# Performance work log

Measured on AMD Instinct MI355X. Metric: run time of the kernel, lower is better.

Reference implementation:

```python
import jax, jax.numpy as jnp
import numpy as np

T, B = 256, 64
X_DIM, H_DIM, Z_DIM = 128, 1024, 128


def _lin(k, out_d, in_d):
    return jax.random.normal(k, (out_d, in_d), jnp.float32) * 0.05


def setup_inputs() -> dict:
    key = jax.random.key(0)
    ks = jax.random.split(key, 18)
    return {
        "x": jax.random.normal(ks[0], (T, B, X_DIM), jnp.float32),
        "y": jax.random.uniform(ks[1], (T, B, X_DIM), jnp.float32),
        "eps": jax.random.normal(ks[2], (T, B, Z_DIM), jnp.float32),
        # hidden_state_rnn: GRU(x_dim -> h_dim), bias=False
        "h_Wih": _lin(ks[3], 3 * H_DIM, X_DIM),
        "h_Whh": _lin(ks[4], 3 * H_DIM, H_DIM),
        # rnn: GRU(h_dim + x_dim -> h_dim), bias=False (input is [y_t, h_t])
        "a_Wih": _lin(ks[5], 3 * H_DIM, X_DIM + H_DIM),
        "a_Whh": _lin(ks[6], 3 * H_DIM, H_DIM),
        "enc_W1": _lin(ks[7], H_DIM, H_DIM), "enc_b1": jnp.zeros(H_DIM, jnp.float32),
        "enc_W2": _lin(ks[8], H_DIM, H_DIM), "enc_b2": jnp.zeros(H_DIM, jnp.float32),
        "encm_W": _lin(ks[9], Z_DIM, H_DIM), "encm_b": jnp.zeros(Z_DIM, jnp.float32),
        "encs_W": _lin(ks[10], Z_DIM, H_DIM), "encs_b": jnp.zeros(Z_DIM, jnp.float32),
        "pr_W": _lin(ks[11], H_DIM, H_DIM), "pr_b": jnp.zeros(H_DIM, jnp.float32),
        "prm_W": _lin(ks[12], Z_DIM, H_DIM), "prm_b": jnp.zeros(Z_DIM, jnp.float32),
        "prs_W": _lin(ks[13], Z_DIM, H_DIM), "prs_b": jnp.zeros(Z_DIM, jnp.float32),
        "dec_W1": _lin(ks[14], H_DIM, H_DIM + Z_DIM), "dec_b1": jnp.zeros(H_DIM, jnp.float32),
        "dec_W2": _lin(ks[15], H_DIM, H_DIM), "dec_b2": jnp.zeros(H_DIM, jnp.float32),
        "decm_W": _lin(ks[16], X_DIM, H_DIM), "decm_b": jnp.zeros(X_DIM, jnp.float32),
        "decs_W": _lin(ks[17], X_DIM, H_DIM), "decs_b": jnp.zeros(X_DIM, jnp.float32),
    }


def _gru(xs, Wih, Whh):
    """Single-layer PyTorch-style GRU without biases. xs: [T,B,in]. Returns [T,B,H]."""
    h0 = jnp.zeros((xs.shape[1], Whh.shape[1]), xs.dtype)
    def step(h, xt):
        gi = xt @ Wih.T                      # [B, 3H]
        gh = h @ Whh.T                       # [B, 3H]
        ir, iz, inn = jnp.split(gi, 3, axis=-1)
        hr, hz, hn = jnp.split(gh, 3, axis=-1)
        r = jax.nn.sigmoid(ir + hr)
        zg = jax.nn.sigmoid(iz + hz)
        n = jnp.tanh(inn + r * hn)
        h_new = (1.0 - zg) * n + zg * h
        return h_new, h_new
    return jax.lax.scan(step, h0, xs)[1]


def srnn_forward(x, y, eps, h_Wih, h_Whh, a_Wih, a_Whh,
                 enc_W1, enc_b1, enc_W2, enc_b2, encm_W, encm_b, encs_W, encs_b,
                 pr_W, pr_b, prm_W, prm_b, prs_W, prs_b,
                 dec_W1, dec_b1, dec_W2, dec_b2, decm_W, decm_b, decs_W, decs_b):
    h_seq = _gru(x, h_Wih, h_Whh)            # [T,B,H] forward-time states
    # NOTE: original code aliases h_list and reverses it in place, so all later
    # uses of h_list[t] actually see the time-reversed sequence. Reproduce that.
    h_rev = h_seq[::-1]
    y_rev = y[::-1]
    a_rev = _gru(jnp.concatenate([y_rev, h_rev], axis=-1), a_Wih, a_Whh)  # backward GRU
    a_fwd = a_rev[::-1]                      # a at forward time t saw steps t..T-1

    enc = jax.nn.relu(jax.nn.relu(a_fwd @ enc_W1.T + enc_b1) @ enc_W2.T + enc_b2)
    enc_mean = enc @ encm_W.T + encm_b       # [T,B,Z]
    enc_std = jax.nn.softplus(enc @ encs_W.T + encs_b)
    z = eps * enc_std + enc_mean             # reparameterized sample

    pri = jax.nn.relu(h_rev @ pr_W.T + pr_b)  # bug-faithful: reversed h
    prior_mean = pri @ prm_W.T + prm_b
    prior_std = jax.nn.softplus(pri @ prs_W.T + prs_b)

    dec = jax.nn.relu(
        jax.nn.relu(jnp.concatenate([z, h_rev], axis=-1) @ dec_W1.T + dec_b1)
        @ dec_W2.T + dec_b2)
    dec_mean = jax.nn.sigmoid(dec @ decm_W.T + decm_b)  # [T,B,X]
    dec_std = jax.nn.softplus(dec @ decs_W.T + decs_b)

    kld = 0.5 * jnp.sum(
        2.0 * jnp.log(prior_std) - 2.0 * jnp.log(enc_std)
        + (enc_std ** 2 + (enc_mean - prior_mean) ** 2) / prior_std ** 2 - 1.0)
    nll = -jnp.sum(y * jnp.log(dec_mean) + (1.0 - y) * jnp.log(1.0 - dec_mean))
    return kld, nll, enc_mean, enc_std, dec_mean, dec_std


def reference(x, y, eps, h_Wih, h_Whh, a_Wih, a_Whh,
              enc_W1, enc_b1, enc_W2, enc_b2, encm_W, encm_b, encs_W, encs_b,
              pr_W, pr_b, prm_W, prm_b, prs_W, prs_b,
              dec_W1, dec_b1, dec_W2, dec_b2, decm_W, decm_b, decs_W, decs_b):
    return srnn_forward(x, y, eps, h_Wih, h_Whh, a_Wih, a_Whh,
                        enc_W1, enc_b1, enc_W2, enc_b2, encm_W, encm_b, encs_W, encs_b,
                        pr_W, pr_b, prm_W, prm_b, prs_W, prs_b,
                        dec_W1, dec_b1, dec_W2, dec_b2, decm_W, decm_b, decs_W, decs_b)
```

## Files before the change

kernel.cpp:

```cpp
#include <hip/hip_runtime.h>
#include <cstdint>
#include <cstddef>

#define NT   256
#define NB   64
#define XD   128
#define HD   1024
#define ZD   128
#define H3   3072
#define TBM  16384

typedef __attribute__((ext_vector_type(8))) short bf16x8;
typedef __attribute__((ext_vector_type(4))) float f32x4;
typedef __attribute__((ext_vector_type(4))) unsigned int u32x4;

__device__ __forceinline__ unsigned short f2bf(float f){
  unsigned int u = __float_as_uint(f);
  u += 0x7fffu + ((u >> 16) & 1u);
  return (unsigned short)(u >> 16);
}
__device__ __forceinline__ float bf2f(unsigned short h){
  return __uint_as_float(((unsigned int)h) << 16);
}

template<int N>
__device__ __forceinline__ void vwait(){
  asm volatile("s_waitcnt vmcnt(%0)" :: "i"(N) : "memory");
  __builtin_amdgcn_sched_barrier(0);
}

__device__ __forceinline__ float fsigmoid(float x){
  return 1.f / (1.f + __expf(-x));
}
__device__ __forceinline__ float ftanh(float x){
  float xc = fminf(fmaxf(x, -15.f), 15.f);
  float e = __expf(2.f * xc);
  return (e - 1.f) / (e + 1.f);
}

__device__ __forceinline__ void wait_tags(const unsigned int* tags, unsigned int target){
  if (threadIdx.x < 64){
    const unsigned int* p = tags + threadIdx.x * 32;
    for (;;){
      unsigned int v;
      asm volatile("global_load_dword %0, %1, off sc0 sc1\n\ts_waitcnt vmcnt(0)"
                   : "=v"(v) : "v"(p) : "memory");
      if (__all((int)(v >= target))) break;
    }
  }
  __syncthreads();
}

struct CvtArgs { const float* src[17]; };

__global__ void cvt_all(CvtArgs a, unsigned short* wdst, unsigned short* xdst, unsigned short* ydst){
  const long NG = 2572288;
  for (long g = blockIdx.x*blockDim.x + threadIdx.x; g < NG; g += (long)gridDim.x*blockDim.x){
    long i = g * 8;
    const float* s; unsigned short* d;
    if      (i < 393216)  { s=a.src[0]+i;             d=wdst+i; }
    else if (i < 3538944) { s=a.src[1]+(i-393216);    d=wdst+i; }
    else if (i < 7077888) { s=a.src[2]+(i-3538944);   d=wdst+i; }
    else if (i < 10223616){ s=a.src[3]+(i-7077888);   d=wdst+i; }
    else if (i < 11272192){ s=a.src[4]+(i-10223616);  d=wdst+i; }
    else if (i < 12320768){ s=a.src[5]+(i-11272192);  d=wdst+i; }
    else if (i < 12451840){ s=a.src[6]+(i-12320768);  d=wdst+i; }
    else if (i < 12582912){ s=a.src[7]+(i-12451840);  d=wdst+i; }
    else if (i < 13631488){ s=a.src[8]+(i-12582912);  d=wdst+i; }
    else if (i < 13762560){ s=a.src[9]+(i-13631488);  d=wdst+i; }
    else if (i < 13893632){ s=a.src[10]+(i-13762560); d=wdst+i; }
    else if (i < 15073280){ s=a.src[11]+(i-13893632); d=wdst+i; }
    else if (i < 16121856){ s=a.src[12]+(i-15073280); d=wdst+i; }
    else if (i < 16252928){ s=a.src[13]+(i-16121856); d=wdst+i; }
    else if (i < 16384000){ s=a.src[14]+(i-16252928); d=wdst+i; }
    else if (i < 18481152){ s=a.src[15]+(i-16384000); d=xdst+(i-16384000); }
    else                  { s=a.src[16]+(i-18481152); d=ydst+(i-18481152); }
    float4 v0 = *(const float4*)s;
    float4 v1 = *(const float4*)(s + 4);
    u32x4 o;
    o.x = (unsigned int)f2bf(v0.x) | ((unsigned int)f2bf(v0.y) << 16);
    o.y = (unsigned int)f2bf(v0.z) | ((unsigned int)f2bf(v0.w) << 16);
    o.z = (unsigned int)f2bf(v1.x) | ((unsigned int)f2bf(v1.y) << 16);
    o.w = (unsigned int)f2bf(v1.z) | ((unsigned int)f2bf(v1.w) << 16);
    *(u32x4*)d = o;
  }
}

template<int ACT, int OUT_BF, int BIAS>
__launch_bounds__(256)
__global__ void gemm_bf16(const unsigned short* __restrict__ A1, int rev1, int K1,
                          const unsigned short* __restrict__ A2, int rev2, int K,
                          const unsigned short* __restrict__ W,
                          const float* __restrict__ bias,
                          void* __restrict__ Cv, int N, int m0)
{
  __shared__ __align__(16) unsigned short As[128][40];
  __shared__ __align__(16) unsigned short Ws[128][40];
  const int tid   = threadIdx.x;
  const int mbase = blockIdx.y * 128;
  const int nbase = blockIdx.x * 128;
  const int wid = tid >> 6, lane = tid & 63;
  const int wr = wid >> 1, wc = wid & 1;
  const int fr = lane & 15;
  const int kc = (lane >> 4) * 8;
  const int K2 = K - K1;
  const int nk = K >> 5;

  f32x4 acc[4][4];
  #pragma unroll
  for (int i = 0; i < 4; ++i)
    #pragma unroll
    for (int j = 0; j < 4; ++j)
      acc[i][j] = (f32x4){0.f, 0.f, 0.f, 0.f};

  for (int ks = 0; ks < nk; ++ks){
    const int k0 = ks << 5;
    __syncthreads();
    for (int l = tid; l < 512; l += 256){
      int row = l >> 2, c = l & 3;
      int kk = k0 + c*8;
      int m = m0 + mbase + row;
      uint4 v;
      if (kk < K1){
        int mm = rev1 ? (((255 - (m >> 6)) << 6) | (m & 63)) : m;
        v = *(const uint4*)(A1 + (size_t)mm * K1 + kk);
      } else {
        int mm = rev2 ? (((255 - (m >> 6)) << 6) | (m & 63)) : m;
        v = *(const uint4*)(A2 + (size_t)mm * K2 + (kk - K1));
      }
      *(uint4*)&As[row][c*8] = v;
    }
    for (int l = tid; l < 512; l += 256){
      int row = l >> 2, c = l & 3;
      uint4 v = *(const uint4*)(W + (size_t)(nbase + row) * K + k0 + c*8);
      *(uint4*)&Ws[row][c*8] = v;
    }
    __syncthreads();
    bf16x8 af[4], bfm[4];
    #pragma unroll
    for (int f = 0; f < 4; ++f) af[f]  = *(const bf16x8*)&As[wr*64 + f*16 + fr][kc];
    #pragma unroll
    for (int f = 0; f < 4; ++f) bfm[f] = *(const bf16x8*)&Ws[wc*64 + f*16 + fr][kc];
    #pragma unroll
    for (int i = 0; i < 4; ++i)
      #pragma unroll
      for (int j = 0; j < 4; ++j)
        acc[i][j] = __builtin_amdgcn_mfma_f32_16x16x32_bf16(af[i], bfm[j], acc[i][j], 0, 0, 0);
  }

  #pragma unroll
  for (int i = 0; i < 4; ++i){
    #pragma unroll
    for (int j = 0; j < 4; ++j){
      #pragma unroll
      for (int r = 0; r < 4; ++r){
        int row = mbase + wr*64 + i*16 + (lane >> 4)*4 + r;
        int col = nbase + wc*64 + j*16 + fr;
        float v = acc[i][j][r];
        if (BIAS) v += bias[col];
        if (ACT == 1) v = fmaxf(v, 0.f);
        else if (ACT == 2) v = 1.f / (1.f + expf(-v));
        else if (ACT == 3) v = (v > 20.f) ? v : log1pf(expf(v));
        if (OUT_BF) ((unsigned short*)Cv)[(size_t)row * N + col] = f2bf(v);
        else        ((float*)Cv)[(size_t)row * N + col] = v;
      }
    }
  }
}

__device__ void gemm_gi_tile(char* smem,
                             const unsigned short* __restrict__ A1, int rev1, int K1,
                             const unsigned short* __restrict__ A2, int rev2, int K,
                             const unsigned short* __restrict__ W,
                             unsigned short* __restrict__ C, int m0, int bx, int by)
{
  unsigned short (*As)[40] = (unsigned short(*)[40])smem;
  unsigned short (*Ws)[40] = (unsigned short(*)[40])(smem + 10240);
  const int tid   = threadIdx.x;
  const int mbase = by * 128;
  const int nbase = bx * 128;
  const int wid = tid >> 6, lane = tid & 63;
  const int wr = wid >> 1, wc = wid & 1;
  const int fr = lane & 15;
  const int kc = (lane >> 4) * 8;
  const int K2 = K - K1;
  const int nk = K >> 5;

  f32x4 acc[4][4];
  #pragma unroll
  for (int i = 0; i < 4; ++i)
    #pragma unroll
    for (int j = 0; j < 4; ++j)
      acc[i][j] = (f32x4){0.f, 0.f, 0.f, 0.f};

  for (int ks = 0; ks < nk; ++ks){
    const int k0 = ks << 5;
    __syncthreads();
    for (int l = tid; l < 512; l += 256){
      int row = l >> 2, c = l & 3;
      int kk = k0 + c*8;
      int m = m0 + mbase + row;
      uint4 v;
      if (kk < K1){
        int mm = rev1 ? (((255 - (m >> 6)) << 6) | (m & 63)) : m;
        v = *(const uint4*)(A1 + (size_t)mm * K1 + kk);
      } else {
        int mm = rev2 ? (((255 - (m >> 6)) << 6) | (m & 63)) : m;
        v = *(const uint4*)(A2 + (size_t)mm * K2 + (kk - K1));
      }
      *(uint4*)&As[row][c*8] = v;
    }
    for (int l = tid; l < 512; l += 256){
      int row = l >> 2, c = l & 3;
      uint4 v = *(const uint4*)(W + (size_t)(nbase + row) * K + k0 + c*8);
      *(uint4*)&Ws[row][c*8] = v;
    }
    __syncthreads();
    bf16x8 af[4], bfm[4];
    #pragma unroll
    for (int f = 0; f < 4; ++f) af[f]  = *(const bf16x8*)&As[wr*64 + f*16 + fr][kc];
    #pragma unroll
    for (int f = 0; f < 4; ++f) bfm[f] = *(const bf16x8*)&Ws[wc*64 + f*16 + fr][kc];
    #pragma unroll
    for (int i = 0; i < 4; ++i)
      #pragma unroll
      for (int j = 0; j < 4; ++j)
        acc[i][j] = __builtin_amdgcn_mfma_f32_16x16x32_bf16(af[i], bfm[j], acc[i][j], 0, 0, 0);
  }

  #pragma unroll
  for (int i = 0; i < 4; ++i){
    #pragma unroll
    for (int j = 0; j < 4; ++j){
      #pragma unroll
      for (int r = 0; r < 4; ++r){
        int row = mbase + wr*64 + i*16 + (lane >> 4)*4 + r;
        int col = nbase + wc*64 + j*16 + fr;
        C[(size_t)row * H3 + col] = f2bf(acc[i][j][r]);
      }
    }
  }
  __syncthreads();
}

__device__ void gru_body(char* smem,
                         const unsigned short* __restrict__ W3,
                         const unsigned short* __restrict__ gi,
                         unsigned short* __restrict__ seq,
                         float* __restrict__ hstate,
                         unsigned int* __restrict__ tags,
                         int t0, int dir, int out_off, int nsteps)
{
  uint4 (*Wf)[3][64] = (uint4(*)[3][64])smem;
  unsigned short (*hb2)[16] = (unsigned short(*)[16])(smem + 98304);
  unsigned int* scnt = (unsigned int*)(smem + 100352);
  const int tid  = threadIdx.x;
  const int bid  = blockIdx.x;
  const int c0   = bid * 16;
  const int wid  = tid >> 6, lane = tid & 63;
  const int fr   = lane & 15, q = lane >> 4;
  const int rowb = wid*16 + q*4;
  const int arow = wid*16 + fr;

  for (int ks = wid*8; ks < wid*8 + 8; ++ks)
    #pragma unroll
    for (int g = 0; g < 3; ++g)
      Wf[ks][g][lane] = *(const uint4*)(W3 + (size_t)(g*HD + c0 + fr)*HD + ks*32 + q*8);
  if (tid == 0) *scnt = 0u;

  float hc[4];
  if (t0 == 0){
    hc[0] = hc[1] = hc[2] = hc[3] = 0.f;
  } else {
    #pragma unroll
    for (int r = 0; r < 4; ++r)
      hc[r] = hstate[(size_t)(rowb + r)*HD + c0 + fr];
  }
  __syncthreads();

  for (int tt = 0; tt < nsteps; ++tt){
    const int t = t0 + tt;

    unsigned short g_ir[4], g_iz[4], g_in[4];
    {
      const unsigned short* gb = gi + (size_t)tt*NB*H3;
      #pragma unroll
      for (int r = 0; r < 4; ++r){
        const unsigned short* p = gb + (size_t)(rowb + r)*H3 + c0 + fr;
        g_ir[r] = p[0];
        g_iz[r] = p[HD];
        g_in[r] = p[2*HD];
      }
    }

    f32x4 aR = (f32x4){0.f,0.f,0.f,0.f};
    f32x4 aZ = (f32x4){0.f,0.f,0.f,0.f};
    f32x4 aN = (f32x4){0.f,0.f,0.f,0.f};

    if (t > 0){
      if (tt >= 1) wait_tags(tags, (unsigned int)tt);
      const unsigned short* hp = seq + (size_t)(out_off + dir*(t-1))*NB*HD
                                     + (size_t)arow*HD + q*8;
      u32x4 A[32];
      #pragma unroll
      for (int ks = 0; ks < 32; ++ks)
        asm volatile("global_load_dwordx4 %0, %1, off offset:%2"
                     : "=v"(A[ks]) : "v"(hp), "i"(ks*64));
      #pragma unroll
      for (int b4 = 0; b4 < 4; ++b4){
        if (b4 == 0) vwait<24>();
        else if (b4 == 1) vwait<16>();
        else if (b4 == 2) vwait<8>();
        else vwait<0>();
        #pragma unroll
        for (int k8 = 0; k8 < 8; ++k8){
          const int ks = b4*8 + k8;
          bf16x8 a = *(const bf16x8*)&A[ks];
          aR = __builtin_amdgcn_mfma_f32_16x16x32_bf16(a, *(const bf16x8*)&Wf[ks][0][lane], aR, 0, 0, 0);
          aZ = __builtin_amdgcn_mfma_f32_16x16x32_bf16(a, *(const bf16x8*)&Wf[ks][1][lane], aZ, 0, 0, 0);
          aN = __builtin_amdgcn_mfma_f32_16x16x32_bf16(a, *(const bf16x8*)&Wf[ks][2][lane], aN, 0, 0, 0);
        }
      }
    }

    #pragma unroll
    for (int r = 0; r < 4; ++r){
      float rr = fsigmoid(bf2f(g_ir[r]) + aR[r]);
      float zz = fsigmoid(bf2f(g_iz[r]) + aZ[r]);
      float nn = ftanh(bf2f(g_in[r]) + rr * aN[r]);
      hc[r] = (1.f - zz) * nn + zz * hc[r];
      hb2[rowb + r][fr] = f2bf(hc[r]);
    }
    __syncthreads();
    {
      int row = tid >> 2, c4 = (tid & 3) * 4;
      unsigned long long v = *(const unsigned long long*)&hb2[row][c4];
      unsigned long long* dst = (unsigned long long*)(seq + (size_t)(out_off + dir*t)*NB*HD
                                                          + (size_t)row*HD + c0 + c4);
      (void)__hip_atomic_exchange(dst, v, __ATOMIC_RELAXED, __HIP_MEMORY_SCOPE_AGENT);
    }
    if (tt < nsteps - 1){
      vwait<0>();
      if (lane == 0){
        unsigned int old = atomicAdd(scnt, 1u);
        if (old == (unsigned int)(4*tt + 3))
          (void)__hip_atomic_exchange(tags + bid*32, (unsigned int)(tt + 1),
                                      __ATOMIC_RELAXED, __HIP_MEMORY_SCOPE_AGENT);
      }
    }
  }

  #pragma unroll
  for (int r = 0; r < 4; ++r)
    hstate[(size_t)(rowb + r)*HD + c0 + fr] = hc[r];
}

__global__ __launch_bounds__(256, 1)
void gru_seq(const unsigned short* __restrict__ W3, const unsigned short* __restrict__ gi,
             unsigned short* __restrict__ seq, float* __restrict__ hstate,
             unsigned int* __restrict__ tags, int t0, int dir, int out_off, int nsteps)
{
  __shared__ __align__(16) char smem[100608];
  gru_body(smem, W3, gi, seq, hstate, tags, t0, dir, out_off, nsteps);
}

__global__ __launch_bounds__(256, 1)
void gru_fat(const unsigned short* __restrict__ W3, const unsigned short* __restrict__ gi,
             unsigned short* __restrict__ seq, float* __restrict__ hstate,
             unsigned int* __restrict__ tags, int t0, int dir, int out_off, int nsteps,
             const unsigned short* __restrict__ gA1, int grev1, int gK1,
             const unsigned short* __restrict__ gA2, int grev2, int gK,
             const unsigned short* __restrict__ gW, unsigned short* __restrict__ gC, int gm0)
{
  __shared__ __align__(16) char smem[100608];
  if (blockIdx.x < 64){
    gru_body(smem, W3, gi, seq, hstate, tags, t0, dir, out_off, nsteps);
  } else {
    for (int tl = blockIdx.x - 64; tl < 768; tl += 192)
      gemm_gi_tile(smem, gA1, grev1, gK1, gA2, grev2, gK, gW, gC, gm0, tl % 24, tl / 24);
  }
}

__global__ void z_make(const float* __restrict__ eps, const float* __restrict__ em,
                       const float* __restrict__ es, unsigned short* __restrict__ zb, int n){
  for (int i = blockIdx.x*blockDim.x + threadIdx.x; i < n; i += gridDim.x*blockDim.x)
    zb[i] = f2bf(eps[i] * es[i] + em[i]);
}

__global__ void kld_partial(const float* __restrict__ em, const float* __restrict__ es,
                            const float* __restrict__ pm, const float* __restrict__ ps,
                            float* __restrict__ part, int n){
  float s = 0.f;
  for (int i = blockIdx.x*blockDim.x + threadIdx.x; i < n; i += gridDim.x*blockDim.x){
    float e = es[i], p = ps[i], d = em[i] - pm[i];
    s += 2.f*(logf(p) - logf(e)) + (e*e + d*d)/(p*p) - 1.f;
  }
  __shared__ float red[256];
  red[threadIdx.x] = s; __syncthreads();
  for (int off = 128; off; off >>= 1){
    if (threadIdx.x < off) red[threadIdx.x] += red[threadIdx.x + off];
    __syncthreads();
  }
  if (threadIdx.x == 0) part[blockIdx.x] = red[0];
}

__global__ void nll_partial(const float* __restrict__ y, const float* __restrict__ dm,
                            float* __restrict__ part, int n){
  float s = 0.f;
  for (int i = blockIdx.x*blockDim.x + threadIdx.x; i < n; i += gridDim.x*blockDim.x){
    float yy = y[i], d = dm[i];
    s += yy * logf(d) + (1.f - yy) * logf(1.f - d);
  }
  __shared__ float red[256];
  red[threadIdx.x] = s; __syncthreads();
  for (int off = 128; off; off >>= 1){
    if (threadIdx.x < off) red[threadIdx.x] += red[threadIdx.x + off];
    __syncthreads();
  }
  if (threadIdx.x == 0) part[blockIdx.x] = red[0];
}

__global__ void final_sum(const float* __restrict__ part, int n, float scale, float* __restrict__ out){
  float s = 0.f;
  for (int i = threadIdx.x; i < n; i += 256) s += part[i];
  __shared__ float red[256];
  red[threadIdx.x] = s; __syncthreads();
  for (int off = 128; off; off >>= 1){
    if (threadIdx.x < off) red[threadIdx.x] += red[threadIdx.x + off];
    __syncthreads();
  }
  if (threadIdx.x == 0) out[0] = scale * red[0];
}

extern "C" void kernel_launch(void* const* d_in, const int* in_sizes, int n_in,
                              void* d_out, int out_size, void* d_ws, size_t ws_size,
                              hipStream_t stream)
{
  const float* y   = (const float*)d_in[1];
  const float* eps = (const float*)d_in[2];
  const float* enc_b1 = (const float*)d_in[8];
  const float* enc_b2 = (const float*)d_in[10];
  const float* encm_b = (const float*)d_in[12];
  const float* encs_b = (const float*)d_in[14];
  const float* pr_b   = (const float*)d_in[16];
  const float* prm_b  = (const float*)d_in[18];
  const float* prs_b  = (const float*)d_in[20];
  const float* dec_b1 = (const float*)d_in[22];
  const float* dec_b2 = (const float*)d_in[24];
  const float* decm_b = (const float*)d_in[26];
  const float* decs_b = (const float*)d_in[28];

  char* ws = (char*)d_ws;
  size_t off = 0;
  auto alloc = [&](size_t bytes){ size_t o = off; off += (bytes + 255) & ~(size_t)255; return o; };
  const size_t o_big   = alloc((size_t)71303168);
  const size_t o_hseq  = alloc((size_t)TBM * HD * 2);
  const size_t o_aseq  = alloc((size_t)TBM * HD * 2);
  const size_t o_wbf   = alloc((size_t)16384000 * 2);
  const size_t o_hst   = alloc((size_t)NB * HD * 4);
  const size_t o_bar   = alloc((size_t)65536);
  const size_t o_pkld  = alloc((size_t)1024 * 4);
  const size_t o_pnll  = alloc((size_t)1024 * 4);
  (void)off; (void)ws_size;

  char* big = ws + o_big;
  unsigned short* gihA = (unsigned short*)(big);
  unsigned short* gihB = (unsigned short*)(big + 25165824);
  unsigned short* xbf  = (unsigned short*)(big + 50331648);
  unsigned short* ybf  = (unsigned short*)(big + 54525952);
  unsigned short* tA  = (unsigned short*)(big);
  unsigned short* tB  = (unsigned short*)(big + 33554432);
  unsigned short* zbf = (unsigned short*)(big + 67108864);

  unsigned short* hseq = (unsigned short*)(ws + o_hseq);
  unsigned short* aseq = (unsigned short*)(ws + o_aseq);
  unsigned short* wbf  = (unsigned short*)(ws + o_wbf);
  float* hstate = (float*)(ws + o_hst);
  unsigned int* bar = (unsigned int*)(ws + o_bar);
  float* pkld = (float*)(ws + o_pkld);
  float* pnll = (float*)(ws + o_pnll);

  const int widx[15] = {3,4,5,6,7,9,11,13,15,17,19,21,23,25,27};
  const size_t wsz[15] = {393216,3145728,3538944,3145728,1048576,1048576,131072,131072,
                          1048576,131072,131072,1179648,1048576,131072,131072};
  size_t woff[15]; { size_t a = 0; for (int i = 0; i < 15; ++i){ woff[i] = a; a += wsz[i]; } }
  unsigned short* w_hWih = wbf + woff[0];
  unsigned short* w_hWhh = wbf + woff[1];
  unsigned short* w_aWih = wbf + woff[2];
  unsigned short* w_aWhh = wbf + woff[3];
  unsigned short* w_enc1 = wbf + woff[4];
  unsigned short* w_enc2 = wbf + woff[5];
  unsigned short* w_encm = wbf + woff[6];
  unsigned short* w_encs = wbf + woff[7];
  unsigned short* w_pr   = wbf + woff[8];
  unsigned short* w_prm  = wbf + woff[9];
  unsigned short* w_prs  = wbf + woff[10];
  unsigned short* w_dec1 = wbf + woff[11];
  unsigned short* w_dec2 = wbf + woff[12];
  unsigned short* w_decm = wbf + woff[13];
  unsigned short* w_decs = wbf + woff[14];

  float* out = (float*)d_out;
  float* em_out = out + 2;
  float* es_out = out + 2 + 2097152;
  float* dm_out = out + 2 + 2*2097152;
  float* ds_out = out + 2 + 3*2097152;
  float* pm = dm_out;
  float* ps = ds_out;

  CvtArgs ca;
  for (int i = 0; i < 15; ++i) ca.src[i] = (const float*)d_in[widx[i]];
  ca.src[15] = (const float*)d_in[0];
  ca.src[16] = (const float*)d_in[1];
  cvt_all<<<2048, 256, 0, stream>>>(ca, wbf, xbf, ybf);
  (void)hipMemsetAsync(bar, 0, 65536, stream);

  const dim3 blk(256);
  const dim3 gQ3072(24, 32);
  const dim3 g1024(HD/128, TBM/128);
  const dim3 g128(1, TBM/128);
  const unsigned short* nul = (const unsigned short*)nullptr;

  gemm_bf16<0,1,0><<<gQ3072, blk, 0, stream>>>(xbf, 0, XD, nul, 0, XD, w_hWih, nullptr, gihA, H3, 0);
  gru_fat<<<256, blk, 0, stream>>>(w_hWhh, gihA, hseq, hstate, bar + 0*2048, 0,   +1, 0, 64,
                                   xbf, 0, XD, nul, 0, XD, w_hWih, gihB, 4096);
  gru_fat<<<256, blk, 0, stream>>>(w_hWhh, gihB, hseq, hstate, bar + 1*2048, 64,  +1, 0, 64,
                                   xbf, 0, XD, nul, 0, XD, w_hWih, gihA, 8192);
  gru_fat<<<256, blk, 0, stream>>>(w_hWhh, gihA, hseq, hstate, bar + 2*2048, 128, +1, 0, 64,
                                   xbf, 0, XD, nul, 0, XD, w_hWih, gihB, 12288);
  gru_seq<<<64, blk, 0, stream>>>(w_hWhh, gihB, hseq, hstate, bar + 3*2048, 192, +1, 0, 64);

  gemm_bf16<0,1,0><<<gQ3072, blk, 0, stream>>>(ybf, 1, XD, hseq, 1, XD + HD, w_aWih, nullptr, gihA, H3, 0);
  gru_fat<<<256, blk, 0, stream>>>(w_aWhh, gihA, aseq, hstate, bar + 4*2048, 0,   -1, 255, 64,
                                   ybf, 1, XD, hseq, 1, XD + HD, w_aWih, gihB, 4096);
  gru_fat<<<256, blk, 0, stream>>>(w_aWhh, gihB, aseq, hstate, bar + 5*2048, 64,  -1, 255, 64,
                                   ybf, 1, XD, hseq, 1, XD + HD, w_aWih, gihA, 8192);
  gru_fat<<<256, blk, 0, stream>>>(w_aWhh, gihA, aseq, hstate, bar + 6*2048, 128, -1, 255, 64,
                                   ybf, 1, XD, hseq, 1, XD + HD, w_aWih, gihB, 12288);
  gru_seq<<<64, blk, 0, stream>>>(w_aWhh, gihB, aseq, hstate, bar + 7*2048, 192, -1, 255, 64);

  gemm_bf16<1,1,1><<<g1024, blk, 0, stream>>>(aseq, 0, HD, nul, 0, HD, w_enc1, enc_b1, tA, HD, 0);
  gemm_bf16<1,1,1><<<g1024, blk, 0, stream>>>(tA, 0, HD, nul, 0, HD, w_enc2, enc_b2, tB, HD, 0);
  gemm_bf16<0,0,1><<<g128, blk, 0, stream>>>(tB, 0, HD, nul, 0, HD, w_encm, encm_b, em_out, ZD, 0);
  gemm_bf16<3,0,1><<<g128, blk, 0, stream>>>(tB, 0, HD, nul, 0, HD, w_encs, encs_b, es_out, ZD, 0);
  z_make<<<2048, 256, 0, stream>>>(eps, em_out, es_out, zbf, TBM*ZD);

  gemm_bf16<1,1,1><<<g1024, blk, 0, stream>>>(hseq, 1, HD, nul, 1, HD, w_pr, pr_b, tA, HD, 0);
  gemm_bf16<0,0,1><<<g128, blk, 0, stream>>>(tA, 0, HD, nul, 0, HD, w_prm, prm_b, pm, ZD, 0);
  gemm_bf16<3,0,1><<<g128, blk, 0, stream>>>(tA, 0, HD, nul, 0, HD, w_prs, prs_b, ps, ZD, 0);
  kld_partial<<<1024, 256, 0, stream>>>(em_out, es_out, pm, ps, pkld, TBM*ZD);
  final_sum<<<1, 256, 0, stream>>>(pkld, 1024, 0.5f, out + 0);

  gemm_bf16<1,1,1><<<g1024, blk, 0, stream>>>(zbf, 0, ZD, hseq, 1, ZD + HD, w_dec1, dec_b1, tA, HD, 0);
  gemm_bf16<1,1,1><<<g1024, blk, 0, stream>>>(tA, 0, HD, nul, 0, HD, w_dec2, dec_b2, tB, HD, 0);
  gemm_bf16<2,0,1><<<g128, blk, 0, stream>>>(tB, 0, HD, nul, 0, HD, w_decm, decm_b, dm_out, ZD, 0);
  gemm_bf16<3,0,1><<<g128, blk, 0, stream>>>(tB, 0, HD, nul, 0, HD, w_decs, decs_b, ds_out, ZD, 0);

  nll_partial<<<1024, 256, 0, stream>>>(y, dm_out, pnll, TBM*XD);
  final_sum<<<1, 256, 0, stream>>>(pnll, 1024, -1.0f, out + 1);
}
```

Baseline: 4.839 ms.

## Pipeline tag polling, simplify GRU step signaling, shrink fat grids, fuse head GEMMs

```diff
diff --git a/kernel.cpp b/kernel.cpp
--- a/kernel.cpp
+++ b/kernel.cpp
@@ -41,12 +41,22 @@
 __device__ __forceinline__ void wait_tags(const unsigned int* tags, unsigned int target){
   if (threadIdx.x < 64){
     const unsigned int* p = tags + threadIdx.x * 32;
+    unsigned int a, b;
+    asm volatile("global_load_dword %0, %2, off sc0 sc1\n\t"
+                 "global_load_dword %1, %2, off sc0 sc1"
+                 : "=v"(a), "=v"(b) : "v"(p) : "memory");
     for (;;){
-      unsigned int v;
-      asm volatile("global_load_dword %0, %1, off sc0 sc1\n\ts_waitcnt vmcnt(0)"
-                   : "=v"(v) : "v"(p) : "memory");
-      if (__all((int)(v >= target))) break;
-    }
+      asm volatile("s_waitcnt vmcnt(1)" ::: "memory");
+      __builtin_amdgcn_sched_barrier(0);
+      if (__all((int)(a >= target))) break;
+      asm volatile("global_load_dword %0, %1, off sc0 sc1" : "=v"(a) : "v"(p) : "memory");
+      asm volatile("s_waitcnt vmcnt(1)" ::: "memory");
+      __builtin_amdgcn_sched_barrier(0);
+      if (__all((int)(b >= target))) break;
+      asm volatile("global_load_dword %0, %1, off sc0 sc1" : "=v"(b) : "v"(p) : "memory");
+    }
+    asm volatile("s_waitcnt vmcnt(0)" ::: "memory");
+    __builtin_amdgcn_sched_barrier(0);
   }
   __syncthreads();
 }
@@ -168,6 +178,77 @@
   }
 }
 
+template<int ACTA, int ACTB>
+__launch_bounds__(256)
+__global__ void gemm_dual(const unsigned short* __restrict__ A,
+                          const unsigned short* __restrict__ Wa, const float* __restrict__ ba,
+                          float* __restrict__ Ca,
+                          const unsigned short* __restrict__ Wb, const float* __restrict__ bb,
+                          float* __restrict__ Cb)
+{
+  const unsigned short* W = blockIdx.x ? Wb : Wa;
+  const float* bias = blockIdx.x ? bb : ba;
+  float* C = blockIdx.x ? Cb : Ca;
+  const int act = blockIdx.x ? ACTB : ACTA;
+
+  __shared__ __align__(16) unsigned short As[128][40];
+  __shared__ __align__(16) unsigned short Ws[128][40];
+  const int tid   = threadIdx.x;
+  const int mbase = blockIdx.y * 128;
+  const int wid = tid >> 6, lane = tid & 63;
+  const int wr = wid >> 1, wc = wid & 1;
+  const int fr = lane & 15;
+  const int kc = (lane >> 4) * 8;
+
+  f32x4 acc[4][4];
+  #pragma unroll
+  for (int i = 0; i < 4; ++i)
+    #pragma unroll
+    for (int j = 0; j < 4; ++j)
+      acc[i][j] = (f32x4){0.f, 0.f, 0.f, 0.f};
+
+  for (int ks = 0; ks < 32; ++ks){
+    const int k0 = ks << 5;
+    __syncthreads();
+    for (int l = tid; l < 512; l += 256){
+      int row = l >> 2, c = l & 3;
+      *(uint4*)&As[row][c*8] = *(const uint4*)(A + (size_t)(mbase + row) * HD + k0 + c*8);
+    }
+    for (int l = tid; l < 512; l += 256){
+      int row = l >> 2, c = l & 3;
+      *(uint4*)&Ws[row][c*8] = *(const uint4*)(W + (size_t)row * HD + k0 + c*8);
+    }
+    __syncthreads();
+    bf16x8 af[4], bfm[4];
+    #pragma unroll
+    for (int f = 0; f < 4; ++f) af[f]  = *(const bf16x8*)&As[wr*64 + f*16 + fr][kc];
+    #pragma unroll
+    for (int f = 0; f < 4; ++f) bfm[f] = *(const bf16x8*)&Ws[wc*64 + f*16 + fr][kc];
+    #pragma unroll
+    for (int i = 0; i < 4; ++i)
+      #pragma unroll
+      for (int j = 0; j < 4; ++j)
+        acc[i][j] = __builtin_amdgcn_mfma_f32_16x16x32_bf16(af[i], bfm[j], acc[i][j], 0, 0, 0);
+  }
+
+  #pragma unroll
+  for (int i = 0; i < 4; ++i){
+    #pragma unroll
+    for (int j = 0; j < 4; ++j){
+      #pragma unroll
+      for (int r = 0; r < 4; ++r){
+        int row = mbase + wr*64 + i*16 + (lane >> 4)*4 + r;
+        int col = wc*64 + j*16 + fr;
+        float v = acc[i][j][r] + bias[col];
+        if (act == 1) v = fmaxf(v, 0.f);
+        else if (act == 2) v = 1.f / (1.f + expf(-v));
+        else if (act == 3) v = (v > 20.f) ? v : log1pf(expf(v));
+        C[(size_t)row * ZD + col] = v;
+      }
+    }
+  }
+}
+
 __device__ void gemm_gi_tile(char* smem,
                              const unsigned short* __restrict__ A1, int rev1, int K1,
                              const unsigned short* __restrict__ A2, int rev2, int K,
@@ -253,7 +334,6 @@
 {
   uint4 (*Wf)[3][64] = (uint4(*)[3][64])smem;
   unsigned short (*hb2)[16] = (unsigned short(*)[16])(smem + 98304);
-  unsigned int* scnt = (unsigned int*)(smem + 100352);
   const int tid  = threadIdx.x;
   const int bid  = blockIdx.x;
   const int c0   = bid * 16;
@@ -266,7 +346,6 @@
     #pragma unroll
     for (int g = 0; g < 3; ++g)
       Wf[ks][g][lane] = *(const uint4*)(W3 + (size_t)(g*HD + c0 + fr)*HD + ks*32 + q*8);
-  if (tid == 0) *scnt = 0u;
 
   float hc[4];
   if (t0 == 0){
@@ -341,12 +420,10 @@
     }
     if (tt < nsteps - 1){
       vwait<0>();
-      if (lane == 0){
-        unsigned int old = atomicAdd(scnt, 1u);
-        if (old == (unsigned int)(4*tt + 3))
-          (void)__hip_atomic_exchange(tags + bid*32, (unsigned int)(tt + 1),
-                                      __ATOMIC_RELAXED, __HIP_MEMORY_SCOPE_AGENT);
-      }
+      __syncthreads();
+      if (tid == 0)
+        (void)__hip_atomic_exchange(tags + bid*32, (unsigned int)(tt + 1),
+                                    __ATOMIC_RELAXED, __HIP_MEMORY_SCOPE_AGENT);
     }
   }
 
@@ -376,7 +453,7 @@
   if (blockIdx.x < 64){
     gru_body(smem, W3, gi, seq, hstate, tags, t0, dir, out_off, nsteps);
   } else {
-    for (int tl = blockIdx.x - 64; tl < 768; tl += 192)
+    for (int tl = blockIdx.x - 64; tl < 768; tl += 96)
       gemm_gi_tile(smem, gA1, grev1, gK1, gA2, grev2, gK, gW, gC, gm0, tl % 24, tl / 24);
   }
 }
@@ -518,43 +595,40 @@
   const dim3 blk(256);
   const dim3 gQ3072(24, 32);
   const dim3 g1024(HD/128, TBM/128);
-  const dim3 g128(1, TBM/128);
+  const dim3 gDual(2, TBM/128);
   const unsigned short* nul = (const unsigned short*)nullptr;
 
   gemm_bf16<0,1,0><<<gQ3072, blk, 0, stream>>>(xbf, 0, XD, nul, 0, XD, w_hWih, nullptr, gihA, H3, 0);
-  gru_fat<<<256, blk, 0, stream>>>(w_hWhh, gihA, hseq, hstate, bar + 0*2048, 0,   +1, 0, 64,
+  gru_fat<<<160, blk, 0, stream>>>(w_hWhh, gihA, hseq, hstate, bar + 0*2048, 0,   +1, 0, 64,
                                    xbf, 0, XD, nul, 0, XD, w_hWih, gihB, 4096);
-  gru_fat<<<256, blk, 0, stream>>>(w_hWhh, gihB, hseq, hstate, bar + 1*2048, 64,  +1, 0, 64,
+  gru_fat<<<160, blk, 0, stream>>>(w_hWhh, gihB, hseq, hstate, bar + 1*2048, 64,  +1, 0, 64,
                                    xbf, 0, XD, nul, 0, XD, w_hWih, gihA, 8192);
-  gru_fat<<<256, blk, 0, stream>>>(w_hWhh, gihA, hseq, hstate, bar + 2*2048, 128, +1, 0, 64,
+  gru_fat<<<160, blk, 0, stream>>>(w_hWhh, gihA, hseq, hstate, bar + 2*2048, 128, +1, 0, 64,
                                    xbf, 0, XD, nul, 0, XD, w_hWih, gihB, 12288);
   gru_seq<<<64, blk, 0, stream>>>(w_hWhh, gihB, hseq, hstate, bar + 3*2048, 192, +1, 0, 64);
 
   gemm_bf16<0,1,0><<<gQ3072, blk, 0, stream>>>(ybf, 1, XD, hseq, 1, XD + HD, w_aWih, nullptr, gihA, H3, 0);
-  gru_fat<<<256, blk, 0, stream>>>(w_aWhh, gihA, aseq, hstate, bar + 4*2048, 0,   -1, 255, 64,
+  gru_fat<<<160, blk, 0, stream>>>(w_aWhh, gihA, aseq, hstate, bar + 4*2048, 0,   -1, 255, 64,
                                    ybf, 1, XD, hseq, 1, XD + HD, w_aWih, gihB, 4096);
-  gru_fat<<<256, blk, 0, stream>>>(w_aWhh, gihB, aseq, hstate, bar + 5*2048, 64,  -1, 255, 64,
+  gru_fat<<<160, blk, 0, stream>>>(w_aWhh, gihB, aseq, hstate, bar + 5*2048, 64,  -1, 255, 64,
                                    ybf, 1, XD, hseq, 1, XD + HD, w_aWih, gihA, 8192);
-  gru_fat<<<256, blk, 0, stream>>>(w_aWhh, gihA, aseq, hstate, bar + 6*2048, 128, -1, 255, 64,
+  gru_fat<<<160, blk, 0, stream>>>(w_aWhh, gihA, aseq, hstate, bar + 6*2048, 128, -1, 255, 64,
                                    ybf, 1, XD, hseq, 1, XD + HD, w_aWih, gihB, 12288);
   gru_seq<<<64, blk, 0, stream>>>(w_aWhh, gihB, aseq, hstate, bar + 7*2048, 192, -1, 255, 64);
 
   gemm_bf16<1,1,1><<<g1024, blk, 0, stream>>>(aseq, 0, HD, nul, 0, HD, w_enc1, enc_b1, tA, HD, 0);
   gemm_bf16<1,1,1><<<g1024, blk, 0, stream>>>(tA, 0, HD, nul, 0, HD, w_enc2, enc_b2, tB, HD, 0);
-  gemm_bf16<0,0,1><<<g128, blk, 0, stream>>>(tB, 0, HD, nul, 0, HD, w_encm, encm_b, em_out, ZD, 0);
-  gemm_bf16<3,0,1><<<g128, blk, 0, stream>>>(tB, 0, HD, nul, 0, HD, w_encs, encs_b, es_out, ZD, 0);
+  gemm_dual<0,3><<<gDual, blk, 0, stream>>>(tB, w_encm, encm_b, em_out, w_encs, encs_b, es_out);
   z_make<<<2048, 256, 0, stream>>>(eps, em_out, es_out, zbf, TBM*ZD);
 
   gemm_bf16<1,1,1><<<g1024, blk, 0, stream>>>(hseq, 1, HD, nul, 1, HD, w_pr, pr_b, tA, HD, 0);
-  gemm_bf16<0,0,1><<<g128, blk, 0, stream>>>(tA, 0, HD, nul, 0, HD, w_prm, prm_b, pm, ZD, 0);
-  gemm_bf16<3,0,1><<<g128, blk, 0, stream>>>(tA, 0, HD, nul, 0, HD, w_prs, prs_b, ps, ZD, 0);
+  gemm_dual<0,3><<<gDual, blk, 0, stream>>>(tA, w_prm, prm_b, pm, w_prs, prs_b, ps);
   kld_partial<<<1024, 256, 0, stream>>>(em_out, es_out, pm, ps, pkld, TBM*ZD);
   final_sum<<<1, 256, 0, stream>>>(pkld, 1024, 0.5f, out + 0);
 
   gemm_bf16<1,1,1><<<g1024, blk, 0, stream>>>(zbf, 0, ZD, hseq, 1, ZD + HD, w_dec1, dec_b1, tA, HD, 0);
   gemm_bf16<1,1,1><<<g1024, blk, 0, stream>>>(tA, 0, HD, nul, 0, HD, w_dec2, dec_b2, tB, HD, 0);
-  gemm_bf16<2,0,1><<<g128, blk, 0, stream>>>(tB, 0, HD, nul, 0, HD, w_decm, decm_b, dm_out, ZD, 0);
-  gemm_bf16<3,0,1><<<g128, blk, 0, stream>>>(tB, 0, HD, nul, 0, HD, w_decs, decs_b, ds_out, ZD, 0);
+  gemm_dual<2,3><<<gDual, blk, 0, stream>>>(tB, w_decm, decm_b, dm_out, w_decs, decs_b, ds_out);
 
   nll_partial<<<1024, 256, 0, stream>>>(y, dm_out, pnll, TBM*XD);
   final_sum<<<1, 256, 0, stream>>>(pnll, 1024, -1.0f, out + 1);
```

Result: faster. 4.633 ms (-4.3%).
